# Optimization experiments

Measured on AMD Instinct MI355X. Metric: run time of the kernel, lower is better.

Reference implementation:

```python
import jax, jax.numpy as jnp
import numpy as np

N_NODES = 100000
N_EDGES = 1600000
DIM = 64
N_GRAPHS = 1000


def setup_inputs() -> dict:
    key = jax.random.key(0)
    ks = jax.random.split(key, 6)
    s = 1.0 / np.sqrt(DIM)
    x = jax.random.normal(ks[0], (N_NODES, DIM), dtype=jnp.float32)
    edge_index = jax.random.randint(ks[1], (2, N_EDGES), 0, N_NODES, dtype=jnp.int64)
    batch = jnp.sort(jax.random.randint(ks[2], (N_NODES,), 0, N_GRAPHS, dtype=jnp.int64))
    W1 = jax.random.normal(ks[3], (DIM, DIM), dtype=jnp.float32) * s
    b1 = jnp.zeros((DIM,), jnp.float32)
    W2 = jax.random.normal(ks[4], (DIM, DIM), dtype=jnp.float32) * s
    b2 = jnp.zeros((DIM,), jnp.float32)
    return {"x": x, "W1": W1, "b1": b1, "W2": W2, "b2": b2,
            "edge_index": edge_index, "batch": batch}


def reference(x, W1, b1, W2, b2, edge_index, batch):
    n = x.shape[0]
    loop = jnp.arange(n, dtype=edge_index.dtype)
    src = jnp.concatenate([edge_index[0], loop])  # [E+N] with self-loops
    dst = jnp.concatenate([edge_index[1], loop])
    # symmetric GCN normalization: deg^{-1/2}[src] * deg^{-1/2}[dst]
    deg = jax.ops.segment_sum(jnp.ones(src.shape[0], x.dtype), dst, num_segments=n)
    dinv = jax.lax.rsqrt(jnp.maximum(deg, 1.0))  # deg >= 1 due to self-loops
    norm = (dinv[src] * dinv[dst])[:, None]      # [E+N, 1]

    def gcn(h, W, b):
        h = h @ W                                  # transform first (smaller dim path)
        msg = h[src] * norm                        # gather + normalize
        return jax.ops.segment_sum(msg, dst, num_segments=n) + b

    h = jax.nn.relu(gcn(x, W1, b1))
    # dropout: eval mode -> identity
    h = jax.nn.relu(gcn(h, W2, b2))

    counts = jax.ops.segment_sum(jnp.ones((n,), x.dtype), batch, num_segments=N_GRAPHS)
    pooled = jax.ops.segment_sum(h, batch, num_segments=N_GRAPHS)
    return pooled / jnp.maximum(counts, 1.0)[:, None]
```

## Files before the change

kernel.cpp:

```cpp
#include <hip/hip_runtime.h>
#include <hip/hip_fp16.h>

#define DIM 64
#define BIN_SHIFT 7
#define BINSZ 128
#define MAXBINS 1024
#define PB 512
#define PB_LOG 9

typedef __attribute__((ext_vector_type(2))) float floatx2;


__global__ __launch_bounds__(256) void k_hist(const int* __restrict__ dst,
                                              int* __restrict__ C, int E, int NB) {
    __shared__ int h[MAXBINS];
    for (int i = threadIdx.x; i < NB; i += 256) h[i] = 0;
    __syncthreads();
    int per = (E + PB - 1) / PB;
    int e0 = blockIdx.x * per;
    int e1 = e0 + per; if (e1 > E) e1 = E;
    for (int e = e0 + (int)threadIdx.x; e < e1; e += 256)
        atomicAdd(&h[dst[e] >> BIN_SHIFT], 1);
    __syncthreads();
    for (int i = threadIdx.x; i < NB; i += 256)
        C[blockIdx.x * NB + i] = h[i];
}


__global__ __launch_bounds__(1024) void k_scanA(const int* __restrict__ C,
                                                int* __restrict__ S,
                                                int* __restrict__ bsums, int NB, int M) {
    __shared__ int sh[1024];
    int tid = threadIdx.x;
    int j0 = blockIdx.x * 4096 + tid * 4;
    int v[4]; int sum = 0;
#pragma unroll
    for (int t = 0; t < 4; ++t) {
        int j = j0 + t; int x = 0;
        if (j < M) { int bin = j >> PB_LOG, blk = j & (PB - 1); x = C[blk * NB + bin]; }
        v[t] = sum; sum += x;
    }
    sh[tid] = sum;
    __syncthreads();
#pragma unroll
    for (int d = 1; d < 1024; d <<= 1) {
        int t = (tid >= d) ? sh[tid - d] : 0;
        __syncthreads();
        sh[tid] += t;
        __syncthreads();
    }
    int excl = sh[tid] - sum;
#pragma unroll
    for (int t = 0; t < 4; ++t) {
        int j = j0 + t;
        if (j < M) S[j] = excl + v[t];
    }
    if (tid == 1023) bsums[blockIdx.x] = sh[1023];
}


__global__ __launch_bounds__(1024) void k_scanB(int* __restrict__ bsums, int nb) {
    __shared__ int s[1024];
    int tid = threadIdx.x;
    int v = (tid < nb) ? bsums[tid] : 0;
    s[tid] = v;
    __syncthreads();
#pragma unroll
    for (int d = 1; d < 1024; d <<= 1) {
        int t = (tid >= d) ? s[tid - d] : 0;
        __syncthreads();
        s[tid] += t;
        __syncthreads();
    }
    if (tid < nb) bsums[tid] = s[tid] - v;
}


__global__ __launch_bounds__(256) void k_bucket(const int* __restrict__ src,
                                                const int* __restrict__ dst,
                                                const int* __restrict__ S,
                                                const int* __restrict__ bsums,
                                                int* __restrict__ bkt, int E, int NB) {
    __shared__ int lcur[MAXBINS];
    int blk = blockIdx.x;
    for (int i = threadIdx.x; i < NB; i += 256) {
        int j = i * PB + blk;
        lcur[i] = S[j] + bsums[j >> 12];
    }
    __syncthreads();
    int per = (E + PB - 1) / PB;
    int e0 = blk * per;
    int e1 = e0 + per; if (e1 > E) e1 = E;
    for (int e = e0 + (int)threadIdx.x; e < e1; e += 256) {
        int d = dst[e];
        int pos = atomicAdd(&lcur[d >> BIN_SHIFT], 1);
        bkt[pos] = src[e] | ((d & (BINSZ - 1)) << 24);
    }
}


__global__ __launch_bounds__(256) void k_binsort(const int* __restrict__ bkt,
                                                 const int* __restrict__ S,
                                                 const int* __restrict__ bsums,
                                                 int* __restrict__ csr,
                                                 int* __restrict__ off,
                                                 float* __restrict__ dinv,
                                                 const int* __restrict__ batch,
                                                 int* __restrict__ goff,
                                                 int* __restrict__ nperm,
                                                 int N, int G, int E, int NB) {
    __shared__ int cnt[BINSZ], bas[BINSZ], cur[BINSZ];
    __shared__ int wsum[4];
    int tid = threadIdx.x;
    int b = blockIdx.x;
    int j0 = b << PB_LOG;
    int s0 = S[j0] + bsums[j0 >> 12];
    int s1 = E;
    if (b + 1 < NB) { int j1 = (b + 1) << PB_LOG; s1 = S[j1] + bsums[j1 >> 12]; }
    if (tid < BINSZ) { cnt[tid] = 0; cur[tid] = 0; }
    __syncthreads();
    for (int i = s0 + tid; i < s1; i += 256)
        atomicAdd(&cnt[(bkt[i] >> 24) & (BINSZ - 1)], 1);
    __syncthreads();
    int my = (tid < BINSZ) ? cnt[tid] : 0;
    int lane = tid & 63, wv = tid >> 6;
    int x = my;
#pragma unroll
    for (int d = 1; d < 64; d <<= 1) {
        int t = __shfl_up(x, d);
        if (lane >= d) x += t;
    }
    if (lane == 63) wsum[wv] = x;
    __syncthreads();
    int prefix = 0;
    for (int w = 0; w < wv; ++w) prefix += wsum[w];
    int ex = x + prefix - my;
    if (tid < BINSZ) {
        bas[tid] = ex;
        int v = (b << BIN_SHIFT) + tid;
        if (v < N) {
            off[v] = s0 + ex;
            dinv[v] = rsqrtf((float)(my + 1));
            if (v == N - 1) off[N] = E;
            int bb = batch[v];
            int prev = (v == 0) ? -1 : batch[v - 1];
            for (int g = prev + 1; g <= bb; ++g) goff[g] = v;
            if (v == N - 1)
                for (int g = bb + 1; g <= G; ++g) goff[g] = N;
        }
    }
    if (tid < BINSZ) {
        int v = (b << BIN_SHIFT) + tid;
        if (v < N) {
            int nvalid = N - (b << BIN_SHIFT);
            if (nvalid > BINSZ) nvalid = BINSZ;
            int d = my, rk = 0;
            for (int j = 0; j < nvalid; ++j) {
                int dj = cnt[j];
                rk += (int)((dj < d) || (dj == d && j < tid));
            }
            nperm[(b << BIN_SHIFT) + rk] = v;
        } else {
            nperm[v] = N;
        }
    }
    __syncthreads();
    for (int i = s0 + tid; i < s1; i += 256) {
        int p = bkt[i];
        int lo = (p >> 24) & (BINSZ - 1);
        int li = atomicAdd(&cur[lo], 1);
        csr[s0 + bas[lo] + li] = p & 0xFFFFFF;
    }
}


__global__ __launch_bounds__(256) void k_gemm(const float* __restrict__ Xf,
                                              const float* __restrict__ W,
                                              const float* __restrict__ dinv,
                                              unsigned int* __restrict__ Y8, int N) {
    __shared__ float Ws[64 * 64];
    __shared__ float Xs[16 * 64];
    int tid = threadIdx.x;
#pragma unroll
    for (int i = 0; i < 16; ++i) Ws[tid + 256 * i] = W[tid + 256 * i];

    int row0 = blockIdx.x * 16;
    int r = tid >> 4, c4 = (tid & 15) << 2;
    int row = row0 + r;
    {
        float4 v = make_float4(0.f, 0.f, 0.f, 0.f);
        if (row < N) v = *(const float4*)(Xf + (size_t)row * DIM + c4);
        *(float4*)(Xs + r * DIM + c4) = v;
    }
    __syncthreads();

    float4 acc = make_float4(0.f, 0.f, 0.f, 0.f);
#pragma unroll
    for (int k = 0; k < 64; ++k) {
        float xk = Xs[r * DIM + k];
        float4 w = *(const float4*)(Ws + k * DIM + c4);
        acc.x += xk * w.x; acc.y += xk * w.y;
        acc.z += xk * w.z; acc.w += xk * w.w;
    }
    if (row < N) {
        float s = dinv[row];
        int p = 0;
        p = __builtin_amdgcn_cvt_pk_fp8_f32(acc.x * s, acc.y * s, p, false);
        p = __builtin_amdgcn_cvt_pk_fp8_f32(acc.z * s, acc.w * s, p, true);
        Y8[(size_t)row * 16 + (c4 >> 2)] = (unsigned int)p;
    } else if (row == N) {
        Y8[(size_t)row * 16 + (c4 >> 2)] = 0u;
    }
}


__device__ __forceinline__ float4 gather_rows(const unsigned int* __restrict__ hs8,
                                              const int* __restrict__ csr,
                                              int k0, int k1, int v, int l, int gw4,
                                              int N) {
    float4 a0, a1, a2, a3;
    {
        unsigned int u = hs8[(unsigned)((v << 4) | l)];
        floatx2 f0 = __builtin_amdgcn_cvt_pk_f32_fp8((int)u, false);
        floatx2 f1 = __builtin_amdgcn_cvt_pk_f32_fp8((int)u, true);
        a0 = make_float4(f0.x, f0.y, f1.x, f1.y);
        a1 = make_float4(0.f, 0.f, 0.f, 0.f);
        a2 = make_float4(0.f, 0.f, 0.f, 0.f);
        a3 = make_float4(0.f, 0.f, 0.f, 0.f);
    }
    for (int kb = k0; kb < k1; kb += 16) {
        int rem = k1 - kb;
        int idx = (l < rem) ? csr[kb + l] : N;
        int mm = rem < 16 ? rem : 16;
        for (int j = 0; j < mm; j += 8) {
            int s0 = __shfl(idx, gw4 + j + 0);
            int s1 = __shfl(idx, gw4 + j + 1);
            int s2 = __shfl(idx, gw4 + j + 2);
            int s3 = __shfl(idx, gw4 + j + 3);
            int s4 = __shfl(idx, gw4 + j + 4);
            int s5 = __shfl(idx, gw4 + j + 5);
            int s6 = __shfl(idx, gw4 + j + 6);
            int s7 = __shfl(idx, gw4 + j + 7);
            unsigned int u0 = hs8[(unsigned)((s0 << 4) | l)];
            unsigned int u1 = hs8[(unsigned)((s1 << 4) | l)];
            unsigned int u2 = hs8[(unsigned)((s2 << 4) | l)];
            unsigned int u3 = hs8[(unsigned)((s3 << 4) | l)];
            unsigned int u4 = hs8[(unsigned)((s4 << 4) | l)];
            unsigned int u5 = hs8[(unsigned)((s5 << 4) | l)];
            unsigned int u6 = hs8[(unsigned)((s6 << 4) | l)];
            unsigned int u7 = hs8[(unsigned)((s7 << 4) | l)];
            floatx2 p0l = __builtin_amdgcn_cvt_pk_f32_fp8((int)u0, false);
            floatx2 p0h = __builtin_amdgcn_cvt_pk_f32_fp8((int)u0, true);
            floatx2 p1l = __builtin_amdgcn_cvt_pk_f32_fp8((int)u1, false);
            floatx2 p1h = __builtin_amdgcn_cvt_pk_f32_fp8((int)u1, true);
            floatx2 p2l = __builtin_amdgcn_cvt_pk_f32_fp8((int)u2, false);
            floatx2 p2h = __builtin_amdgcn_cvt_pk_f32_fp8((int)u2, true);
            floatx2 p3l = __builtin_amdgcn_cvt_pk_f32_fp8((int)u3, false);
            floatx2 p3h = __builtin_amdgcn_cvt_pk_f32_fp8((int)u3, true);
            floatx2 p4l = __builtin_amdgcn_cvt_pk_f32_fp8((int)u4, false);
            floatx2 p4h = __builtin_amdgcn_cvt_pk_f32_fp8((int)u4, true);
            floatx2 p5l = __builtin_amdgcn_cvt_pk_f32_fp8((int)u5, false);
            floatx2 p5h = __builtin_amdgcn_cvt_pk_f32_fp8((int)u5, true);
            floatx2 p6l = __builtin_amdgcn_cvt_pk_f32_fp8((int)u6, false);
            floatx2 p6h = __builtin_amdgcn_cvt_pk_f32_fp8((int)u6, true);
            floatx2 p7l = __builtin_amdgcn_cvt_pk_f32_fp8((int)u7, false);
            floatx2 p7h = __builtin_amdgcn_cvt_pk_f32_fp8((int)u7, true);
            a0.x += p0l.x; a0.y += p0l.y; a0.z += p0h.x; a0.w += p0h.y;
            a1.x += p1l.x; a1.y += p1l.y; a1.z += p1h.x; a1.w += p1h.y;
            a2.x += p2l.x; a2.y += p2l.y; a2.z += p2h.x; a2.w += p2h.y;
            a3.x += p3l.x; a3.y += p3l.y; a3.z += p3h.x; a3.w += p3h.y;
            a0.x += p4l.x; a0.y += p4l.y; a0.z += p4h.x; a0.w += p4h.y;
            a1.x += p5l.x; a1.y += p5l.y; a1.z += p5h.x; a1.w += p5h.y;
            a2.x += p6l.x; a2.y += p6l.y; a2.z += p6h.x; a2.w += p6h.y;
            a3.x += p7l.x; a3.y += p7l.y; a3.z += p7h.x; a3.w += p7h.y;
        }
    }
    return make_float4(a0.x + a1.x + a2.x + a3.x,
                       a0.y + a1.y + a2.y + a3.y,
                       a0.z + a1.z + a2.z + a3.z,
                       a0.w + a1.w + a2.w + a3.w);
}


__global__ __launch_bounds__(256) void k_gather_gemm(const unsigned int* __restrict__ hs8,
                                                     const int* __restrict__ csr,
                                                     const int* __restrict__ off,
                                                     const int* __restrict__ nperm,
                                                     const float* __restrict__ dinv,
                                                     const float* __restrict__ bias,
                                                     const float* __restrict__ W,
                                                     unsigned int* __restrict__ hs_out,
                                                     int N) {
    __shared__ float Ws[64 * 64];
    __shared__ float Xs[16 * 64];
    int tid = threadIdx.x;
#pragma unroll
    for (int i = 0; i < 16; ++i) Ws[tid + 256 * i] = W[tid + 256 * i];
    if (blockIdx.x == 0 && tid < 16)
        hs_out[(size_t)N * 16 + tid] = 0u;

    int r = tid >> 4;
    int l = tid & 15;
    int gw4 = ((tid >> 4) & 3) << 4;
    int v = nperm[blockIdx.x * 16 + r];

    float dv = 0.f;
    float4 h = make_float4(0.f, 0.f, 0.f, 0.f);
    if (v < N) {
        dv = dinv[v];
        float4 bv = ((const float4*)bias)[l];
        float4 acc = gather_rows(hs8, csr, off[v], off[v + 1], v, l, gw4, N);
        h.x = fmaxf(acc.x * dv + bv.x, 0.f);
        h.y = fmaxf(acc.y * dv + bv.y, 0.f);
        h.z = fmaxf(acc.z * dv + bv.z, 0.f);
        h.w = fmaxf(acc.w * dv + bv.w, 0.f);
    }
    *(float4*)(Xs + r * DIM + (l << 2)) = h;
    __syncthreads();

    float4 o = make_float4(0.f, 0.f, 0.f, 0.f);
#pragma unroll
    for (int k = 0; k < 64; ++k) {
        float xk = Xs[r * DIM + k];
        float4 w = *(const float4*)(Ws + k * DIM + (l << 2));
        o.x += xk * w.x; o.y += xk * w.y;
        o.z += xk * w.z; o.w += xk * w.w;
    }
    if (v < N) {
        int p = 0;
        p = __builtin_amdgcn_cvt_pk_fp8_f32(o.x * dv, o.y * dv, p, false);
        p = __builtin_amdgcn_cvt_pk_fp8_f32(o.z * dv, o.w * dv, p, true);
        hs_out[(size_t)v * 16 + l] = (unsigned int)p;
    }
}


__global__ __launch_bounds__(256) void k_gather16(const unsigned int* __restrict__ hs8,
                                                  const int* __restrict__ csr,
                                                  const int* __restrict__ off,
                                                  const int* __restrict__ nperm,
                                                  const float* __restrict__ dinv,
                                                  const float* __restrict__ bias,
                                                  __half* __restrict__ agg, int N) {
    int tid = threadIdx.x;
    int v = nperm[blockIdx.x * 16 + (tid >> 4)];
    if (v >= N) return;
    int l = tid & 15;
    int gw4 = ((tid >> 4) & 3) << 4;
    float dv = dinv[v];
    float4 bv = ((const float4*)bias)[l];
    float4 acc = gather_rows(hs8, csr, off[v], off[v + 1], v, l, gw4, N);
    __half2 p0 = __floats2half2_rn(acc.x * dv + bv.x, acc.y * dv + bv.y);
    __half2 p1 = __floats2half2_rn(acc.z * dv + bv.z, acc.w * dv + bv.w);
    uint2 u;
    u.x = *(unsigned int*)&p0;
    u.y = *(unsigned int*)&p1;
    ((uint2*)(agg + (size_t)v * DIM))[l] = u;
}


__global__ __launch_bounds__(256) void k_pool(const __half* __restrict__ agg,
                                              const int* __restrict__ goff,
                                              float* __restrict__ out, int G) {
    int g = blockIdx.x * 4 + (threadIdx.x >> 6);
    if (g >= G) return;
    int lane = threadIdx.x & 63;
    int q = lane >> 4, c = lane & 15;
    const uint2* h2 = (const uint2*)agg;
    int n0 = goff[g], n1 = goff[g + 1];
    float4 acc = make_float4(0.f, 0.f, 0.f, 0.f);
    for (int i = n0 + q; i < n1; i += 4) {
        uint2 u = h2[(size_t)i * 16 + c];
        float2 f0 = __half22float2(*(__half2*)&u.x);
        float2 f1 = __half22float2(*(__half2*)&u.y);
        acc.x += fmaxf(f0.x, 0.f); acc.y += fmaxf(f0.y, 0.f);
        acc.z += fmaxf(f1.x, 0.f); acc.w += fmaxf(f1.y, 0.f);
    }
    acc.x += __shfl_down(acc.x, 32); acc.y += __shfl_down(acc.y, 32);
    acc.z += __shfl_down(acc.z, 32); acc.w += __shfl_down(acc.w, 32);
    acc.x += __shfl_down(acc.x, 16); acc.y += __shfl_down(acc.y, 16);
    acc.z += __shfl_down(acc.z, 16); acc.w += __shfl_down(acc.w, 16);
    if (q == 0) {
        float inv = 1.0f / fmaxf((float)(n1 - n0), 1.0f);
        *(float4*)(out + ((size_t)g << 6) + (c << 2)) =
            make_float4(acc.x * inv, acc.y * inv, acc.z * inv, acc.w * inv);
    }
}


static inline int cdiv(int a, int b) { return (a + b - 1) / b; }

extern "C" void kernel_launch(void* const* d_in, const int* in_sizes, int n_in,
                              void* d_out, int out_size, void* d_ws, size_t ws_size,
                              hipStream_t stream) {
    const float* x   = (const float*)d_in[0];
    const float* W1  = (const float*)d_in[1];
    const float* b1  = (const float*)d_in[2];
    const float* W2  = (const float*)d_in[3];
    const float* b2  = (const float*)d_in[4];
    const int*   ei  = (const int*)d_in[5];
    const int*   bat = (const int*)d_in[6];

    const int N = in_sizes[0] / DIM;
    const int E = in_sizes[5] / 2;
    const int G = out_size / DIM;
    const int NB = cdiv(N, BINSZ);
    const int M  = NB * PB;
    const int* src = ei;
    const int* dst = ei + E;
    float* out = (float*)d_out;

    __half* hs1    = (__half*)d_ws;
    __half* hs2    = hs1 + (size_t)(N + 1) * DIM;
    __half* agg1   = hs2 + (size_t)(N + 1) * DIM;
    float*  dinv   = (float*)(agg1 + (size_t)N * DIM);
    int*    off    = (int*)(dinv + N);
    int*    goff   = off + (N + 1);
    int*    C      = goff + (G + 1);
    int*    S      = C + (size_t)PB * NB;
    int*    bsums  = S + (size_t)PB * NB;
    int*    csr    = bsums + 1024;
    int*    nperm  = csr + E;
    int*    bkt    = (int*)hs1;
    __half* agg2   = hs1;

    k_hist<<<PB, 256, 0, stream>>>(dst, C, E, NB);
    int nb2 = cdiv(M, 4096);
    k_scanA<<<nb2, 1024, 0, stream>>>(C, S, bsums, NB, M);
    k_scanB<<<1, 1024, 0, stream>>>(bsums, nb2);
    k_bucket<<<PB, 256, 0, stream>>>(src, dst, S, bsums, bkt, E, NB);
    k_binsort<<<NB, 256, 0, stream>>>(bkt, S, bsums, csr, off, dinv, bat, goff,
                                      nperm, N, G, E, NB);

    k_gemm<<<cdiv(N + 1, 16), 256, 0, stream>>>(x, W1, dinv, (unsigned int*)hs1, N);

    const int GGRID = NB * (BINSZ / 16);

    k_gather_gemm<<<GGRID, 256, 0, stream>>>((const unsigned int*)hs1, csr, off, nperm,
                                             dinv, b1, W2, (unsigned int*)hs2, N);

    k_gather16<<<GGRID, 256, 0, stream>>>((const unsigned int*)hs2, csr, off, nperm,
                                          dinv, b2, agg2, N);

    k_pool<<<cdiv(G, 4), 256, 0, stream>>>(agg2, goff, out, G);
}
```

Baseline: 232.1 us.

## Use fp16 MFMA for dense transforms and drop degree-sorted node permutation

```diff
diff --git a/kernel.cpp b/kernel.cpp
--- a/kernel.cpp
+++ b/kernel.cpp
@@ -9,6 +9,9 @@
 #define PB_LOG 9
 
 typedef __attribute__((ext_vector_type(2))) float floatx2;
+typedef __attribute__((ext_vector_type(4))) float f32x4;
+typedef __attribute__((ext_vector_type(8))) _Float16 f16x8;
+typedef __attribute__((ext_vector_type(4))) _Float16 f16x4;
 
 
 __global__ __launch_bounds__(256) void k_hist(const int* __restrict__ dst,
@@ -107,7 +110,6 @@
                                                  float* __restrict__ dinv,
                                                  const int* __restrict__ batch,
                                                  int* __restrict__ goff,
-                                                 int* __restrict__ nperm,
                                                  int N, int G, int E, int NB) {
     __shared__ int cnt[BINSZ], bas[BINSZ], cur[BINSZ];
     __shared__ int wsum[4];
@@ -149,21 +151,6 @@
                 for (int g = bb + 1; g <= G; ++g) goff[g] = N;
         }
     }
-    if (tid < BINSZ) {
-        int v = (b << BIN_SHIFT) + tid;
-        if (v < N) {
-            int nvalid = N - (b << BIN_SHIFT);
-            if (nvalid > BINSZ) nvalid = BINSZ;
-            int d = my, rk = 0;
-            for (int j = 0; j < nvalid; ++j) {
-                int dj = cnt[j];
-                rk += (int)((dj < d) || (dj == d && j < tid));
-            }
-            nperm[(b << BIN_SHIFT) + rk] = v;
-        } else {
-            nperm[v] = N;
-        }
-    }
     __syncthreads();
     for (int i = s0 + tid; i < s1; i += 256) {
         int p = bkt[i];
@@ -174,42 +161,61 @@
 }
 
 
-__global__ __launch_bounds__(256) void k_gemm(const float* __restrict__ Xf,
+__global__ __launch_bounds__(256) void k_gemm(const float* __restrict__ X,
                                               const float* __restrict__ W,
                                               const float* __restrict__ dinv,
                                               unsigned int* __restrict__ Y8, int N) {
-    __shared__ float Ws[64 * 64];
-    __shared__ float Xs[16 * 64];
-    int tid = threadIdx.x;
-#pragma unroll
-    for (int i = 0; i < 16; ++i) Ws[tid + 256 * i] = W[tid + 256 * i];
-
+    __shared__ float Os[16 * 68];
+    int tid = threadIdx.x;
+    int lane = tid & 63, w = tid >> 6;
+    int m = lane & 15, g = lane >> 4;
     int row0 = blockIdx.x * 16;
-    int r = tid >> 4, c4 = (tid & 15) << 2;
-    int row = row0 + r;
+    int row = row0 + m;
+
+    f16x8 B0, B1;
     {
-        float4 v = make_float4(0.f, 0.f, 0.f, 0.f);
-        if (row < N) v = *(const float4*)(Xf + (size_t)row * DIM + c4);
-        *(float4*)(Xs + r * DIM + c4) = v;
-    }
-    __syncthreads();
-
-    float4 acc = make_float4(0.f, 0.f, 0.f, 0.f);
-#pragma unroll
-    for (int k = 0; k < 64; ++k) {
-        float xk = Xs[r * DIM + k];
-        float4 w = *(const float4*)(Ws + k * DIM + c4);
-        acc.x += xk * w.x; acc.y += xk * w.y;
-        acc.z += xk * w.z; acc.w += xk * w.w;
-    }
-    if (row < N) {
-        float s = dinv[row];
+        int n = (w << 4) + m;
+        const float* wp = W + (g << 3) * 64 + n;
+#pragma unroll
+        for (int j = 0; j < 8; ++j) B0[j] = (_Float16)wp[j * 64];
+        wp += 32 * 64;
+#pragma unroll
+        for (int j = 0; j < 8; ++j) B1[j] = (_Float16)wp[j * 64];
+    }
+    f16x8 A0, A1;
+    {
+        float4 u0 = make_float4(0.f, 0.f, 0.f, 0.f), u1 = u0, u2 = u0, u3 = u0;
+        if (row < N) {
+            const float* xp = X + (size_t)row * DIM + (g << 3);
+            u0 = *(const float4*)(xp);
+            u1 = *(const float4*)(xp + 4);
+            u2 = *(const float4*)(xp + 32);
+            u3 = *(const float4*)(xp + 36);
+        }
+        A0[0] = (_Float16)u0.x; A0[1] = (_Float16)u0.y; A0[2] = (_Float16)u0.z; A0[3] = (_Float16)u0.w;
+        A0[4] = (_Float16)u1.x; A0[5] = (_Float16)u1.y; A0[6] = (_Float16)u1.z; A0[7] = (_Float16)u1.w;
+        A1[0] = (_Float16)u2.x; A1[1] = (_Float16)u2.y; A1[2] = (_Float16)u2.z; A1[3] = (_Float16)u2.w;
+        A1[4] = (_Float16)u3.x; A1[5] = (_Float16)u3.y; A1[6] = (_Float16)u3.z; A1[7] = (_Float16)u3.w;
+    }
+    f32x4 acc = {0.f, 0.f, 0.f, 0.f};
+    acc = __builtin_amdgcn_mfma_f32_16x16x32_f16(A0, B0, acc, 0, 0, 0);
+    acc = __builtin_amdgcn_mfma_f32_16x16x32_f16(A1, B1, acc, 0, 0, 0);
+#pragma unroll
+    for (int j = 0; j < 4; ++j)
+        Os[((g << 2) + j) * 68 + (w << 4) + m] = acc[j];
+    __syncthreads();
+
+    int r = tid >> 4, c = tid & 15;
+    int orow = row0 + r;
+    if (orow < N) {
+        float4 o = *(const float4*)(Os + r * 68 + (c << 2));
+        float s = dinv[orow];
         int p = 0;
-        p = __builtin_amdgcn_cvt_pk_fp8_f32(acc.x * s, acc.y * s, p, false);
-        p = __builtin_amdgcn_cvt_pk_fp8_f32(acc.z * s, acc.w * s, p, true);
-        Y8[(size_t)row * 16 + (c4 >> 2)] = (unsigned int)p;
-    } else if (row == N) {
-        Y8[(size_t)row * 16 + (c4 >> 2)] = 0u;
+        p = __builtin_amdgcn_cvt_pk_fp8_f32(o.x * s, o.y * s, p, false);
+        p = __builtin_amdgcn_cvt_pk_fp8_f32(o.z * s, o.w * s, p, true);
+        Y8[(size_t)orow * 16 + c] = (unsigned int)p;
+    } else if (orow == N) {
+        Y8[(size_t)orow * 16 + c] = 0u;
     }
 }
 
@@ -285,24 +291,32 @@
 __global__ __launch_bounds__(256) void k_gather_gemm(const unsigned int* __restrict__ hs8,
                                                      const int* __restrict__ csr,
                                                      const int* __restrict__ off,
-                                                     const int* __restrict__ nperm,
                                                      const float* __restrict__ dinv,
                                                      const float* __restrict__ bias,
                                                      const float* __restrict__ W,
                                                      unsigned int* __restrict__ hs_out,
                                                      int N) {
-    __shared__ float Ws[64 * 64];
-    __shared__ float Xs[16 * 64];
-    int tid = threadIdx.x;
-#pragma unroll
-    for (int i = 0; i < 16; ++i) Ws[tid + 256 * i] = W[tid + 256 * i];
+    __shared__ _Float16 Xs[16 * 72];
+    __shared__ float Os[16 * 68];
+    int tid = threadIdx.x;
+    int r = tid >> 4, l = tid & 15;
+    int lane = tid & 63, w = tid >> 6;
+    int m = lane & 15, g = lane >> 4;
+    int gw4 = (r & 3) << 4;
+    int v = blockIdx.x * 16 + r;
+
+    f16x8 B0, B1;
+    {
+        int n = (w << 4) + m;
+        const float* wp = W + (g << 3) * 64 + n;
+#pragma unroll
+        for (int j = 0; j < 8; ++j) B0[j] = (_Float16)wp[j * 64];
+        wp += 32 * 64;
+#pragma unroll
+        for (int j = 0; j < 8; ++j) B1[j] = (_Float16)wp[j * 64];
+    }
     if (blockIdx.x == 0 && tid < 16)
         hs_out[(size_t)N * 16 + tid] = 0u;
-
-    int r = tid >> 4;
-    int l = tid & 15;
-    int gw4 = ((tid >> 4) & 3) << 4;
-    int v = nperm[blockIdx.x * 16 + r];
 
     float dv = 0.f;
     float4 h = make_float4(0.f, 0.f, 0.f, 0.f);
@@ -315,18 +329,26 @@
         h.z = fmaxf(acc.z * dv + bv.z, 0.f);
         h.w = fmaxf(acc.w * dv + bv.w, 0.f);
     }
-    *(float4*)(Xs + r * DIM + (l << 2)) = h;
-    __syncthreads();
-
-    float4 o = make_float4(0.f, 0.f, 0.f, 0.f);
-#pragma unroll
-    for (int k = 0; k < 64; ++k) {
-        float xk = Xs[r * DIM + k];
-        float4 w = *(const float4*)(Ws + k * DIM + (l << 2));
-        o.x += xk * w.x; o.y += xk * w.y;
-        o.z += xk * w.z; o.w += xk * w.w;
-    }
+    {
+        f16x4 hv;
+        hv[0] = (_Float16)h.x; hv[1] = (_Float16)h.y;
+        hv[2] = (_Float16)h.z; hv[3] = (_Float16)h.w;
+        *(f16x4*)(Xs + r * 72 + (l << 2)) = hv;
+    }
+    __syncthreads();
+
+    f16x8 A0 = *(const f16x8*)(Xs + m * 72 + (g << 3));
+    f16x8 A1 = *(const f16x8*)(Xs + m * 72 + 32 + (g << 3));
+    f32x4 acc2 = {0.f, 0.f, 0.f, 0.f};
+    acc2 = __builtin_amdgcn_mfma_f32_16x16x32_f16(A0, B0, acc2, 0, 0, 0);
+    acc2 = __builtin_amdgcn_mfma_f32_16x16x32_f16(A1, B1, acc2, 0, 0, 0);
+#pragma unroll
+    for (int j = 0; j < 4; ++j)
+        Os[((g << 2) + j) * 68 + (w << 4) + m] = acc2[j];
+    __syncthreads();
+
     if (v < N) {
+        float4 o = *(const float4*)(Os + r * 68 + (l << 2));
         int p = 0;
         p = __builtin_amdgcn_cvt_pk_fp8_f32(o.x * dv, o.y * dv, p, false);
         p = __builtin_amdgcn_cvt_pk_fp8_f32(o.z * dv, o.w * dv, p, true);
@@ -338,12 +360,11 @@
 __global__ __launch_bounds__(256) void k_gather16(const unsigned int* __restrict__ hs8,
                                                   const int* __restrict__ csr,
                                                   const int* __restrict__ off,
-                                                  const int* __restrict__ nperm,
                                                   const float* __restrict__ dinv,
                                                   const float* __restrict__ bias,
                                                   __half* __restrict__ agg, int N) {
     int tid = threadIdx.x;
-    int v = nperm[blockIdx.x * 16 + (tid >> 4)];
+    int v = blockIdx.x * 16 + (tid >> 4);
     if (v >= N) return;
     int l = tid & 15;
     int gw4 = ((tid >> 4) & 3) << 4;
@@ -420,7 +441,6 @@
     int*    S      = C + (size_t)PB * NB;
     int*    bsums  = S + (size_t)PB * NB;
     int*    csr    = bsums + 1024;
-    int*    nperm  = csr + E;
     int*    bkt    = (int*)hs1;
     __half* agg2   = hs1;
 
@@ -429,18 +449,15 @@
     k_scanA<<<nb2, 1024, 0, stream>>>(C, S, bsums, NB, M);
     k_scanB<<<1, 1024, 0, stream>>>(bsums, nb2);
     k_bucket<<<PB, 256, 0, stream>>>(src, dst, S, bsums, bkt, E, NB);
-    k_binsort<<<NB, 256, 0, stream>>>(bkt, S, bsums, csr, off, dinv, bat, goff,
-                                      nperm, N, G, E, NB);
+    k_binsort<<<NB, 256, 0, stream>>>(bkt, S, bsums, csr, off, dinv, bat, goff, N, G, E, NB);
 
     k_gemm<<<cdiv(N + 1, 16), 256, 0, stream>>>(x, W1, dinv, (unsigned int*)hs1, N);
 
-    const int GGRID = NB * (BINSZ / 16);
-
-    k_gather_gemm<<<GGRID, 256, 0, stream>>>((const unsigned int*)hs1, csr, off, nperm,
-                                             dinv, b1, W2, (unsigned int*)hs2, N);
-
-    k_gather16<<<GGRID, 256, 0, stream>>>((const unsigned int*)hs2, csr, off, nperm,
-                                          dinv, b2, agg2, N);
+    k_gather_gemm<<<cdiv(N, 16), 256, 0, stream>>>((const unsigned int*)hs1, csr, off,
+                                                   dinv, b1, W2, (unsigned int*)hs2, N);
+
+    k_gather16<<<cdiv(N, 16), 256, 0, stream>>>((const unsigned int*)hs2, csr, off,
+                                                dinv, b2, agg2, N);
 
     k_pool<<<cdiv(G, 4), 256, 0, stream>>>(agg2, goff, out, G);
 }
```

New measurement: 203.6 us. -12.3%, faster.
